# Performance work log

Measured on AMD Instinct MI355X. Metric: run time of the kernel, lower is better.

## Reference

```python
import jax, jax.numpy as jnp
import numpy as np

BATCH, ENC_IN, D_MODEL, D_STATE = 16, 256, 256, 16


def _mamba_params(key, d, d_conv, prefix):
    di = 2 * d  # expand = 2
    dtr = max(d // 16, 1)  # dt_rank = ceil(d_model/16)
    ks = jax.random.split(key, 6)
    return {
        prefix + '_in_w': jax.random.normal(ks[0], (2 * di, d), jnp.float32) * 0.02,
        prefix + '_conv_w': jax.random.normal(ks[1], (di, d_conv), jnp.float32) * 0.1,
        prefix + '_conv_b': jnp.zeros((di,), jnp.float32),
        prefix + '_xproj_w': jax.random.normal(ks[2], (dtr + 2 * D_STATE, di), jnp.float32) * 0.02,
        prefix + '_dt_w': jax.random.normal(ks[3], (di, dtr), jnp.float32) * 0.02,
        prefix + '_dt_b': jax.random.normal(ks[4], (di,), jnp.float32) * 0.02,
        prefix + '_Alog': jnp.log(jnp.broadcast_to(jnp.arange(1, D_STATE + 1, dtype=jnp.float32), (di, D_STATE))),
        prefix + '_Dp': jnp.ones((di,), jnp.float32),
        prefix + '_out_w': jax.random.normal(ks[5], (d, di), jnp.float32) * 0.02,
    }


def setup_inputs() -> dict:
    key = jax.random.key(0)
    k0, k1, k2, k3 = jax.random.split(key, 4)
    inp = {
        'x': jax.random.normal(k0, (BATCH, ENC_IN, D_MODEL), jnp.float32),
        'ln_g': jnp.ones((D_MODEL,), jnp.float32),
        'ln_b': jnp.zeros((D_MODEL,), jnp.float32),
    }
    inp.update(_mamba_params(k1, D_MODEL, 1, 'mf'))  # channel mixer fwd, d_conv=1
    inp.update(_mamba_params(k2, D_MODEL, 1, 'mb'))  # channel mixer bwd, d_conv=1
    inp.update(_mamba_params(k3, ENC_IN, 4, 'tm'))   # time mixer, d_conv=4
    return inp


def _mamba(x, in_w, conv_w, conv_b, xproj_w, dt_w, dt_b, Alog, Dp, out_w):
    # x: [B, L, d]  -> standard mamba_ssm Mamba block forward
    B, L, d = x.shape
    di = in_w.shape[0] // 2
    dtr = dt_w.shape[1]
    ds = D_STATE
    xz = x @ in_w.T                      # [B, L, 2*di]
    xs, z = xz[..., :di], xz[..., di:]
    # causal depthwise conv1d (pad left d_conv-1, truncate to L)
    K = conv_w.shape[1]
    xp = jnp.pad(xs, ((0, 0), (K - 1, 0), (0, 0)))
    xs = sum(conv_w[:, k] * xp[:, k:k + L, :] for k in range(K)) + conv_b
    xs = jax.nn.silu(xs)
    x_dbl = xs @ xproj_w.T               # [B, L, dtr + 2*ds]
    dt = x_dbl[..., :dtr]
    Bm = x_dbl[..., dtr:dtr + ds]        # [B, L, ds]
    Cm = x_dbl[..., dtr + ds:]           # [B, L, ds]
    delta = jax.nn.softplus(dt @ dt_w.T + dt_b)          # [B, L, di]
    A = -jnp.exp(Alog)                                   # [di, ds]
    dA = jnp.exp(delta[..., None] * A)                   # [B, L, di, ds]
    dBx = delta[..., None] * Bm[:, :, None, :] * xs[..., None]

    def step(h, inp):
        dAt, dBxt, Ct = inp              # [B,di,ds],[B,di,ds],[B,ds]
        h = dAt * h + dBxt
        return h, jnp.einsum('bds,bs->bd', h, Ct)

    h0 = jnp.zeros((B, di, ds), x.dtype)
    _, ys = jax.lax.scan(step, h0, (dA.transpose(1, 0, 2, 3), dBx.transpose(1, 0, 2, 3), Cm.transpose(1, 0, 2)))
    y = ys.transpose(1, 0, 2) + Dp * xs  # [B, L, di]
    y = y * jax.nn.silu(z)
    return y @ out_w.T                   # [B, L, d]


def _ln(x, g, b, eps=1e-5):
    m = x.mean(-1, keepdims=True)
    v = jnp.mean((x - m) ** 2, axis=-1, keepdims=True)
    return (x - m) / jnp.sqrt(v + eps) * g + b


def reference(x, ln_g, ln_b,
              mf_in_w, mf_conv_w, mf_conv_b, mf_xproj_w, mf_dt_w, mf_dt_b, mf_Alog, mf_Dp, mf_out_w,
              mb_in_w, mb_conv_w, mb_conv_b, mb_xproj_w, mb_dt_w, mb_dt_b, mb_Alog, mb_Dp, mb_out_w,
              tm_in_w, tm_conv_w, tm_conv_b, tm_xproj_w, tm_dt_w, tm_dt_b, tm_Alog, tm_Dp, tm_out_w):
    # BiMamba channel mixer
    y_f = _mamba(x, mf_in_w, mf_conv_w, mf_conv_b, mf_xproj_w, mf_dt_w, mf_dt_b, mf_Alog, mf_Dp, mf_out_w)
    y_b = _mamba(jnp.flip(x, axis=1), mb_in_w, mb_conv_w, mb_conv_b, mb_xproj_w, mb_dt_w, mb_dt_b, mb_Alog, mb_Dp, mb_out_w)
    y0 = y_f + jnp.flip(y_b, axis=1) + x
    y0 = _ln(y0, ln_g, ln_b)             # note: source uses norm1 both times
    # time mixer over the feature dimension
    y1 = y0.transpose(0, 2, 1)           # [B, d_model, enc_in]
    y1 = _mamba(y1, tm_in_w, tm_conv_w, tm_conv_b, tm_xproj_w, tm_dt_w, tm_dt_b, tm_Alog, tm_Dp, tm_out_w)
    y1 = y1.transpose(0, 2, 1)
    y2 = y1 * y0 + x
    return _ln(y2, ln_g, ln_b)
```

## Files before the change

kernel.cpp:

```cpp
#include <hip/hip_runtime.h>
#include <hip/hip_bf16.h>

typedef unsigned short u16;
typedef unsigned int   u32;

typedef short frag8 __attribute__((ext_vector_type(8)));
typedef float f32x4 __attribute__((ext_vector_type(4)));
typedef u16   u16x8 __attribute__((ext_vector_type(8)));
typedef u16   u16x4 __attribute__((ext_vector_type(4)));

__device__ __forceinline__ float bfb2f(u16 u) {
    return __uint_as_float(((u32)u) << 16);
}
__device__ __forceinline__ u16 f2bf(float v) {
    const u32 u = __float_as_uint(v);
    return (u16)((u + 0x7FFFu + ((u >> 16) & 1u)) >> 16);
}
__device__ __forceinline__ float silu_(float x) { return x / (1.f + __expf(-x)); }
__device__ __forceinline__ float softplus_fast(float x) {
    return (x > 20.f) ? x : __logf(1.f + __expf(x));
}
__device__ __forceinline__ void gload_lds16(const void* g, void* l) {
    __builtin_amdgcn_global_load_lds(
        (const __attribute__((address_space(1))) void*)g,
        (__attribute__((address_space(3))) void*)l, 16, 0, 0);
}

struct Cvt {
    const void* src[30];
    int dstoff[30];
    int n[30];
    int bstart[31];
};

__global__ __launch_bounds__(256) void convert_k(Cvt c, const u32* probe,
                                                 float* dst, u16* dstb) {
    const bool isb = (*probe != 0x3F800000u);
    const int bi = blockIdx.x;
    int i = 0;
    while (i < 29 && bi >= c.bstart[i + 1]) ++i;
    const int e = (bi - c.bstart[i]) * 256 + (int)threadIdx.x;
    if (e >= c.n[i]) return;
    const float v = isb ? bfb2f(((const u16*)c.src[i])[e])
                        : ((const float*)c.src[i])[e];
    dst[c.dstoff[i] + e]  = v;
    dstb[c.dstoff[i] + e] = f2bf(v);
}

__global__ __launch_bounds__(256, 4) void gemm1_fb_k(
    const u16* __restrict__ Xbf,
    const u16* __restrict__ Wf, const u16* __restrict__ Wb,
    const float* __restrict__ cwf, const float* __restrict__ cbf,
    const float* __restrict__ cwb, const float* __restrict__ cbb,
    u16* __restrict__ XSb_f, u16* __restrict__ XST_f, u16* __restrict__ ZST_f,
    u16* __restrict__ XSb_b, u16* __restrict__ XST_b, u16* __restrict__ ZST_b)
{
    __shared__ u16 Bs[16384];
    u16 (*tile)[136] = (u16(*)[136])Bs;

    const int br = blockIdx.x >> 4;
    const int n0 = (blockIdx.x & 15) * 64;
    const u16* W = br ? Wb : Wf;
    const float* cw = br ? cwb : cwf;
    const float* cb = br ? cbb : cbf;
    u16* XSb = br ? XSb_b : XSb_f;
    u16* XST = br ? XST_b : XST_f;
    u16* ZST = br ? ZST_b : ZST_f;

    const int t = threadIdx.x;
    const int wave = t >> 6, lane = t & 63;
    const int l15 = lane & 15, quad = lane >> 4;
    const int mblk = blockIdx.y * 128;

    {
        const char* Wp = (const char*)(W + (size_t)n0 * 256);
        const int lane16 = lane * 16;
        #pragma unroll
        for (int j = 0; j < 8; ++j) {
            const int s  = wave * 8 + j;
            const int Lb = s * 1024 + lane16;
            const int Ob = Lb ^ (((Lb >> 9) & 7) << 4);
            gload_lds16(Wp + Ob, (char*)Bs + Lb);
        }
    }
    asm volatile("s_waitcnt vmcnt(0)" ::: "memory");
    __syncthreads();

    const int m0w = mblk + wave * 32;
    const u16* arow0 = Xbf + (size_t)(m0w + l15) * 256 + quad * 8;
    const u16* arow1 = arow0 + 16 * 256;
    f32x4 acc[2][4] = {};
    #pragma unroll
    for (int kk = 0; kk < 8; ++kk) {
        const frag8 a0 = *(const frag8*)(arow0 + kk * 32);
        const frag8 a1 = *(const frag8*)(arow1 + kk * 32);
        #pragma unroll
        for (int ni = 0; ni < 4; ++ni) {
            const int bb = ((ni * 16 + l15) * 512 + kk * 64 + quad * 16)
                         ^ ((l15 & 7) << 4);
            const frag8 b = *(const frag8*)((const char*)Bs + bb);
            acc[0][ni] = __builtin_amdgcn_mfma_f32_16x16x32_bf16(a0, b, acc[0][ni], 0, 0, 0);
            acc[1][ni] = __builtin_amdgcn_mfma_f32_16x16x32_bf16(a1, b, acc[1][ni], 0, 0, 0);
        }
    }
    __syncthreads();

    const bool isx = (n0 < 512);
    #pragma unroll
    for (int mi = 0; mi < 2; ++mi) {
        #pragma unroll
        for (int ni = 0; ni < 4; ++ni) {
            const int n = n0 + ni * 16 + l15;
            #pragma unroll
            for (int r = 0; r < 4; ++r) {
                const int ml = wave * 32 + mi * 16 + quad * 4 + r;
                const int m  = mblk + ml;
                const float v = acc[mi][ni][r];
                const float s = isx ? silu_(fmaf(cw[n], v, cb[n])) : silu_(v);
                const u16 sb = f2bf(s);
                if (isx) XSb[(size_t)m * 512 + n] = sb;
                tile[ni * 16 + l15][ml] = sb;
            }
        }
    }
    __syncthreads();

    const int b2 = mblk >> 8;
    const int l0 = mblk & 255;
    const int rown = t >> 2;
    const int cc  = (t & 3) * 32;
    const int dg = isx ? (n0 + rown) : (n0 - 512 + rown);
    u16* dst = (isx ? XST : ZST) + ((size_t)(b2 * 512 + dg)) * 256 + l0 + cc;
    #pragma unroll
    for (int p = 0; p < 4; ++p)
        *(u16x8*)(dst + p * 8) = *(const u16x8*)&tile[rown][cc + p * 8];
}

__global__ __launch_bounds__(256, 4) void gemm1_tm_k(
    const u16* __restrict__ Ab, const u16* __restrict__ Bbg,
    float* __restrict__ TMRAW, u16* __restrict__ ZST)
{
    __shared__ u16 Bs[16384];
    u16 (*tile)[136] = (u16(*)[136])Bs;

    const int t = threadIdx.x;
    const int wave = t >> 6, lane = t & 63;
    const int l15 = lane & 15, quad = lane >> 4;
    const int mblk = blockIdx.y * 128;
    const int n0 = blockIdx.x * 64;

    {
        const char* Wp = (const char*)(Bbg + (size_t)n0 * 256);
        const int lane16 = lane * 16;
        #pragma unroll
        for (int j = 0; j < 8; ++j) {
            const int s  = wave * 8 + j;
            const int Lb = s * 1024 + lane16;
            const int Ob = Lb ^ (((Lb >> 9) & 7) << 4);
            gload_lds16(Wp + Ob, (char*)Bs + Lb);
        }
    }
    asm volatile("s_waitcnt vmcnt(0)" ::: "memory");
    __syncthreads();

    const int m0w = mblk + wave * 32;
    const u16* arow0 = Ab + (size_t)(m0w + l15) * 256 + quad * 8;
    const u16* arow1 = arow0 + 16 * 256;
    f32x4 acc[2][4] = {};
    #pragma unroll
    for (int kk = 0; kk < 8; ++kk) {
        const frag8 a0 = *(const frag8*)(arow0 + kk * 32);
        const frag8 a1 = *(const frag8*)(arow1 + kk * 32);
        #pragma unroll
        for (int ni = 0; ni < 4; ++ni) {
            const int bb = ((ni * 16 + l15) * 512 + kk * 64 + quad * 16)
                         ^ ((l15 & 7) << 4);
            const frag8 b = *(const frag8*)((const char*)Bs + bb);
            acc[0][ni] = __builtin_amdgcn_mfma_f32_16x16x32_bf16(a0, b, acc[0][ni], 0, 0, 0);
            acc[1][ni] = __builtin_amdgcn_mfma_f32_16x16x32_bf16(a1, b, acc[1][ni], 0, 0, 0);
        }
    }

    const bool isx = (n0 < 512);
    if (isx) {
        #pragma unroll
        for (int mi = 0; mi < 2; ++mi) {
            #pragma unroll
            for (int ni = 0; ni < 4; ++ni) {
                const int n = n0 + ni * 16 + l15;
                #pragma unroll
                for (int r = 0; r < 4; ++r) {
                    const int m = mblk + wave * 32 + mi * 16 + quad * 4 + r;
                    TMRAW[(size_t)m * 512 + n] = acc[mi][ni][r];
                }
            }
        }
    } else {
        __syncthreads();
        #pragma unroll
        for (int mi = 0; mi < 2; ++mi) {
            #pragma unroll
            for (int ni = 0; ni < 4; ++ni) {
                #pragma unroll
                for (int r = 0; r < 4; ++r) {
                    const int ml = wave * 32 + mi * 16 + quad * 4 + r;
                    tile[ni * 16 + l15][ml] = f2bf(silu_(acc[mi][ni][r]));
                }
            }
        }
        __syncthreads();
        const int b2 = mblk >> 8;
        const int l0 = mblk & 255;
        const int rown = t >> 2;
        const int cc  = (t & 3) * 32;
        u16* dst = ZST + ((size_t)(b2 * 512 + (n0 - 512) + rown)) * 256 + l0 + cc;
        #pragma unroll
        for (int p = 0; p < 4; ++p)
            *(u16x8*)(dst + p * 8) = *(const u16x8*)&tile[rown][cc + p * 8];
    }
}

__global__ __launch_bounds__(256, 2) void gemm_x_k(
    const u16* __restrict__ A0, const u16* __restrict__ B0, u16* __restrict__ O0,
    const u16* __restrict__ A1, const u16* __restrict__ B1, u16* __restrict__ O1)
{
    __shared__ char AB[81920];
    const int br = blockIdx.z;
    const u16* Ab = br ? A1 : A0;
    const u16* Bb = br ? B1 : B0;
    u16* out = br ? O1 : O0;
    const int t = threadIdx.x;
    const int wave = t >> 6, lane = t & 63;
    const int l15 = lane & 15, quad = lane >> 4;
    const int mblk = blockIdx.y * 64;
    const int n0 = blockIdx.x * 16;

    {
        const char* Ap = (const char*)(Ab + (size_t)mblk * 512);
        const char* Bp = (const char*)(Bb + (size_t)n0 * 512);
        const int lane16 = lane * 16;
        #pragma unroll
        for (int j = 0; j < 16; ++j) {
            const int Lb = (wave * 16 + j) * 1024 + lane16;
            const int Ob = Lb ^ (((Lb >> 10) & 7) << 4);
            gload_lds16(Ap + Ob, AB + Lb);
        }
        #pragma unroll
        for (int j = 0; j < 4; ++j) {
            const int Lb = (wave * 4 + j) * 1024 + lane16;
            const int Ob = Lb ^ (((Lb >> 10) & 7) << 4);
            gload_lds16(Bp + Ob, AB + 65536 + Lb);
        }
    }
    asm volatile("s_waitcnt vmcnt(0)" ::: "memory");
    __syncthreads();

    f32x4 acc = {};
    #pragma unroll
    for (int kk = 0; kk < 16; ++kk) {
        const int aoff = ((wave * 16 + l15) * 1024 + kk * 64 + quad * 16) ^ ((l15 & 7) << 4);
        const int boff = 65536 + ((l15 * 1024 + kk * 64 + quad * 16) ^ ((l15 & 7) << 4));
        const frag8 a = *(const frag8*)(AB + aoff);
        const frag8 b = *(const frag8*)(AB + boff);
        acc = __builtin_amdgcn_mfma_f32_16x16x32_bf16(a, b, acc, 0, 0, 0);
    }
    const int n = n0 + l15;
    const int m0 = mblk + wave * 16;
    #pragma unroll
    for (int r = 0; r < 4; ++r)
        out[(size_t)(m0 + quad * 4 + r) * 48 + n] = f2bf(acc[r]);
}

__global__ __launch_bounds__(256) void gemm_dt_k(
    const u16* __restrict__ A0, const u16* __restrict__ W0,
    const float* __restrict__ bias0, u16* __restrict__ O0,
    const u16* __restrict__ A1, const u16* __restrict__ W1,
    const float* __restrict__ bias1, u16* __restrict__ O1)
{
    __shared__ u16 tile[64][72];
    const int br = blockIdx.z;
    const u16* Ab = br ? A1 : A0;
    const u16* Wt = br ? W1 : W0;
    const float* bias = br ? bias1 : bias0;
    u16* out = br ? O1 : O0;

    const int t = threadIdx.x;
    const int wave = t >> 6, lane = t & 63;
    const int l15 = lane & 15, quad = lane >> 4;
    const int mblk = blockIdx.y * 64;
    const int m0 = mblk + wave * 16;
    const int n0 = blockIdx.x * 64;
    f32x4 acc[4] = {};
    frag8 a;
    #pragma unroll
    for (int j = 0; j < 8; ++j) a[j] = 0;
    if (quad < 2) a = *(const frag8*)(Ab + (size_t)(m0 + l15) * 48 + quad * 8);
    #pragma unroll
    for (int ni = 0; ni < 4; ++ni) {
        frag8 b;
        #pragma unroll
        for (int j = 0; j < 8; ++j) b[j] = 0;
        if (quad < 2) b = *(const frag8*)(Wt + (size_t)(n0 + ni * 16 + l15) * 16 + quad * 8);
        acc[ni] = __builtin_amdgcn_mfma_f32_16x16x32_bf16(a, b, acc[ni], 0, 0, 0);
    }
    #pragma unroll
    for (int ni = 0; ni < 4; ++ni) {
        const int n = n0 + ni * 16 + l15;
        #pragma unroll
        for (int r = 0; r < 4; ++r) {
            const int m = m0 + quad * 4 + r;
            tile[n - n0][m - mblk] = f2bf(softplus_fast(acc[ni][r] + bias[n]));
        }
    }
    __syncthreads();
    const int b  = mblk >> 8;
    const int l0 = mblk & 255;
    const int rown = t >> 2;
    const int chk  = (t & 3) * 16;
    u16* dst = out + ((size_t)(b * 512 + n0 + rown)) * 256 + l0 + chk;
    *(u16x8*)dst       = *(const u16x8*)&tile[rown][chk];
    *(u16x8*)(dst + 8) = *(const u16x8*)&tile[rown][chk + 8];
}

__global__ __launch_bounds__(256, 4) void gemm_o_k(
    const u16* __restrict__ A0, const u16* __restrict__ B0, float* __restrict__ O0,
    const u16* __restrict__ A1, const u16* __restrict__ B1, float* __restrict__ O1)
{
    __shared__ char Bs[32768];
    const int br = blockIdx.z;
    const u16* Ab = br ? A1 : A0;
    const u16* Bb = br ? B1 : B0;
    float* out = br ? O1 : O0;
    const int t = threadIdx.x;
    const int wave = t >> 6, lane = t & 63;
    const int l15 = lane & 15, quad = lane >> 4;
    const int mblk = blockIdx.y * 128;
    const int n0 = blockIdx.x * 32;

    {
        const char* Bp = (const char*)(Bb + (size_t)n0 * 512);
        const int lane16 = lane * 16;
        #pragma unroll
        for (int j = 0; j < 8; ++j) {
            const int Lb = (wave * 8 + j) * 1024 + lane16;
            const int Ob = Lb ^ (((Lb >> 10) & 7) << 4);
            gload_lds16(Bp + Ob, Bs + Lb);
        }
    }
    asm volatile("s_waitcnt vmcnt(0)" ::: "memory");
    __syncthreads();

    const int m0w = mblk + wave * 32;
    const u16* arow0 = Ab + (size_t)(m0w + l15) * 512 + quad * 8;
    const u16* arow1 = arow0 + 16 * 512;
    f32x4 acc[2][2] = {};
    #pragma unroll
    for (int kk = 0; kk < 16; ++kk) {
        const frag8 a0 = *(const frag8*)(arow0 + kk * 32);
        const frag8 a1 = *(const frag8*)(arow1 + kk * 32);
        #pragma unroll
        for (int ni = 0; ni < 2; ++ni) {
            const int boff = ((ni * 16 + l15) * 1024 + kk * 64 + quad * 16) ^ ((l15 & 7) << 4);
            const frag8 b = *(const frag8*)(Bs + boff);
            acc[0][ni] = __builtin_amdgcn_mfma_f32_16x16x32_bf16(a0, b, acc[0][ni], 0, 0, 0);
            acc[1][ni] = __builtin_amdgcn_mfma_f32_16x16x32_bf16(a1, b, acc[1][ni], 0, 0, 0);
        }
    }
    #pragma unroll
    for (int mi = 0; mi < 2; ++mi) {
        #pragma unroll
        for (int ni = 0; ni < 2; ++ni) {
            const int n = n0 + ni * 16 + l15;
            #pragma unroll
            for (int r = 0; r < 4; ++r) {
                const int m = mblk + wave * 32 + mi * 16 + quad * 4 + r;
                out[(size_t)m * 256 + n] = acc[mi][ni][r];
            }
        }
    }
}

__global__ __launch_bounds__(256) void conv4t_k(
    const float* __restrict__ raw, const float* __restrict__ cw, const float* __restrict__ cb,
    u16* __restrict__ XSb, u16* __restrict__ XST)
{
    __shared__ u16 tile[64][72];
    const int b  = blockIdx.y;
    const int c0 = blockIdx.x * 64;
    const int cl = threadIdx.x & 63;
    const int seg = threadIdx.x >> 6;
    const int c = c0 + cl;
    const int tq = blockIdx.z * 64;
    const int tp0 = tq + seg * 16;
    const float w0 = cw[c * 4 + 0], w1 = cw[c * 4 + 1];
    const float w2 = cw[c * 4 + 2], w3 = cw[c * 4 + 3];
    const float bias = cb[c];
    float r3 = 0.f, r2 = 0.f, r1 = 0.f;
    if (tp0 > 0) {
        r3 = raw[((size_t)(b * 256 + tp0 - 3)) * 512 + c];
        r2 = raw[((size_t)(b * 256 + tp0 - 2)) * 512 + c];
        r1 = raw[((size_t)(b * 256 + tp0 - 1)) * 512 + c];
    }
    #pragma unroll
    for (int i = 0; i < 16; ++i) {
        const int tp = tp0 + i;
        const float cur = raw[((size_t)(b * 256 + tp)) * 512 + c];
        float acc = fmaf(w0, r3, bias);
        acc = fmaf(w1, r2, acc);
        acc = fmaf(w2, r1, acc);
        acc = fmaf(w3, cur, acc);
        const u16 sb = f2bf(silu_(acc));
        XSb[((size_t)(b * 256 + tp)) * 512 + c] = sb;
        tile[cl][tp - tq] = sb;
        r3 = r2; r2 = r1; r1 = cur;
    }
    __syncthreads();
    const int row = threadIdx.x >> 2;
    const int ch  = (threadIdx.x & 3) * 16;
    u16* dst = XST + ((size_t)(b * 512 + c0 + row)) * 256 + tq + ch;
    #pragma unroll
    for (int j = 0; j < 4; ++j)
        *(u16x4*)(dst + j * 4) = *(const u16x4*)&tile[row][ch + j * 4];
}

struct ScanSet {
    const u16 *xst, *zst, *dlt, *xdblb;
    const float *Alog, *Dp;
    u16* Y;
};

__global__ __launch_bounds__(256) void scan_fused_k(ScanSet s0, ScanSet s1, int branchStart)
{
    __shared__ float Ps[4354];
    __shared__ float Es[4354];
    const int br  = (blockIdx.x >= (u32)branchStart) ? 1 : 0;
    const ScanSet S = br ? s1 : s0;
    const int rev = br;
    const int bi2 = blockIdx.x - br * branchStart;
    const int b  = bi2 >> 6;
    const int d0 = (bi2 & 63) << 3;
    const int g  = threadIdx.x >> 3;
    const int cl = threadIdx.x & 7;
    const int d  = d0 + cl;

    bool fast = true;
    #pragma unroll
    for (int s = 0; s < 16; ++s) {
        const float a = -__expf(S.Alog[d * 16 + s]);
        fast &= (fabsf(a + (float)(s + 1)) < 1e-3f);
    }

    const size_t crow = ((size_t)(b * 512 + d)) * 256;
    const int lbase = rev ? (248 - g * 8) : (g * 8);
    const u16x8 xs8 = *(const u16x8*)(S.xst + crow + lbase);
    const u16x8 dl8 = *(const u16x8*)(S.dlt + crow + lbase);

    float h[16], P[16];
    #pragma unroll
    for (int s = 0; s < 16; ++s) { h[s] = 0.f; P[s] = 1.f; }
    float e1prod = 1.f;

    #pragma unroll
    for (int i = 0; i < 8; ++i) {
        const int j = rev ? (7 - i) : i;
        const int l = lbase + j;
        const size_t row = (size_t)(b * 256 + l);
        const float dl = bfb2f(dl8[j]);
        const float xv = bfb2f(xs8[j]);
        const u16x8 bv0 = *(const u16x8*)(S.xdblb + row * 48 + 16);
        const u16x8 bv1 = *(const u16x8*)(S.xdblb + row * 48 + 24);
        const float dlx = dl * xv;
        if (fast) {
            const float e1 = __expf(-dl);
            e1prod *= e1;
            const float e2 = e1 * e1, e4 = e2 * e2, e8 = e4 * e4;
            float pw[16];
            pw[0] = e1;        pw[1] = e2;        pw[2] = e2 * e1;   pw[3] = e4;
            pw[4] = e4 * e1;   pw[5] = e4 * e2;   pw[6] = e4 * pw[2]; pw[7] = e8;
            pw[8] = e8 * e1;   pw[9] = e8 * e2;   pw[10] = e8 * pw[2]; pw[11] = e8 * e4;
            pw[12] = e8 * pw[4]; pw[13] = e8 * pw[5]; pw[14] = e8 * pw[6]; pw[15] = e8 * e8;
            #pragma unroll
            for (int s = 0; s < 8; ++s)
                h[s] = fmaf(pw[s], h[s], dlx * bfb2f(bv0[s]));
            #pragma unroll
            for (int s = 8; s < 16; ++s)
                h[s] = fmaf(pw[s], h[s], dlx * bfb2f(bv1[s - 8]));
        } else {
            #pragma unroll
            for (int s = 0; s < 16; ++s) {
                const float As = -__expf(S.Alog[d * 16 + s]);
                const float dA = __expf(dl * As);
                P[s] *= dA;
                const float Bv = bfb2f((s < 8) ? bv0[s] : bv1[s - 8]);
                h[s] = fmaf(dA, h[s], dlx * Bv);
            }
        }
    }
    if (fast) {
        const float e1 = e1prod;
        const float e2 = e1 * e1, e4 = e2 * e2, e8 = e4 * e4;
        P[0] = e1;        P[1] = e2;        P[2] = e2 * e1;   P[3] = e4;
        P[4] = e4 * e1;   P[5] = e4 * e2;   P[6] = e4 * P[2]; P[7] = e8;
        P[8] = e8 * e1;   P[9] = e8 * e2;   P[10] = e8 * P[2]; P[11] = e8 * e4;
        P[12] = e8 * P[4]; P[13] = e8 * P[5]; P[14] = e8 * P[6]; P[15] = e8 * e8;
    }
    const int pbx = (g * 8 + cl) * 17;
    #pragma unroll
    for (int s = 0; s < 16; ++s) { Ps[pbx + s] = P[s]; Es[pbx + s] = h[s]; }
    __syncthreads();

    if (threadIdx.x < 128) {
        const int cl2 = threadIdx.x >> 4, s2 = threadIdx.x & 15;
        float hh = 0.f;
        #pragma unroll
        for (int gg = 0; gg < 32; ++gg) {
            const int o = (gg * 8 + cl2) * 17 + s2;
            const float tmp = Es[o];
            Es[o] = hh;
            hh = fmaf(Ps[o], hh, tmp);
        }
    }
    __syncthreads();

    #pragma unroll
    for (int s = 0; s < 16; ++s) h[s] = Es[pbx + s];
    const float Dpd = S.Dp[d];
    const u16x8 zs8 = *(const u16x8*)(S.zst + crow + lbase);
    #pragma unroll
    for (int i = 0; i < 8; ++i) {
        const int j = rev ? (7 - i) : i;
        const int l = lbase + j;
        const size_t row = (size_t)(b * 256 + l);
        const float dl = bfb2f(dl8[j]);
        const float xv = bfb2f(xs8[j]);
        const float zv = bfb2f(zs8[j]);
        const u16x8 bv0 = *(const u16x8*)(S.xdblb + row * 48 + 16);
        const u16x8 bv1 = *(const u16x8*)(S.xdblb + row * 48 + 24);
        const u16x8 cv0 = *(const u16x8*)(S.xdblb + row * 48 + 32);
        const u16x8 cv1 = *(const u16x8*)(S.xdblb + row * 48 + 40);
        const float dlx = dl * xv;
        float a0 = 0.f, a1 = 0.f, a2 = 0.f, a3 = 0.f;
        if (fast) {
            const float e1 = __expf(-dl);
            const float e2 = e1 * e1, e4 = e2 * e2, e8 = e4 * e4;
            float pw[16];
            pw[0] = e1;        pw[1] = e2;        pw[2] = e2 * e1;   pw[3] = e4;
            pw[4] = e4 * e1;   pw[5] = e4 * e2;   pw[6] = e4 * pw[2]; pw[7] = e8;
            pw[8] = e8 * e1;   pw[9] = e8 * e2;   pw[10] = e8 * pw[2]; pw[11] = e8 * e4;
            pw[12] = e8 * pw[4]; pw[13] = e8 * pw[5]; pw[14] = e8 * pw[6]; pw[15] = e8 * e8;
            #pragma unroll
            for (int s = 0; s < 16; ++s) {
                const float Bv = bfb2f((s < 8) ? bv0[s] : bv1[s - 8]);
                const float Cv = bfb2f((s < 8) ? cv0[s] : cv1[s - 8]);
                h[s] = fmaf(pw[s], h[s], dlx * Bv);
                const float hv = h[s] * Cv;
                if ((s & 3) == 0) a0 += hv;
                else if ((s & 3) == 1) a1 += hv;
                else if ((s & 3) == 2) a2 += hv;
                else a3 += hv;
            }
        } else {
            #pragma unroll
            for (int s = 0; s < 16; ++s) {
                const float As = -__expf(S.Alog[d * 16 + s]);
                const float dA = __expf(dl * As);
                const float Bv = bfb2f((s < 8) ? bv0[s] : bv1[s - 8]);
                const float Cv = bfb2f((s < 8) ? cv0[s] : cv1[s - 8]);
                h[s] = fmaf(dA, h[s], dlx * Bv);
                const float hv = h[s] * Cv;
                if ((s & 3) == 0) a0 += hv;
                else if ((s & 3) == 1) a1 += hv;
                else if ((s & 3) == 2) a2 += hv;
                else a3 += hv;
            }
        }
        const float acc = (a0 + a1) + (a2 + a3);
        S.Y[row * 512 + d] = f2bf((acc + Dpd * xv) * zv);
    }
}

__global__ __launch_bounds__(256) void combine_ln_k(
    const float* __restrict__ YF, const float* __restrict__ YB,
    const float* __restrict__ X, const float* __restrict__ g, const float* __restrict__ bb,
    float* __restrict__ Y0, u16* __restrict__ Y0T)
{
    const int m = blockIdx.x;
    const int c = threadIdx.x;
    const float v = YF[(size_t)m * 256 + c]
                  + YB[(size_t)m * 256 + c]
                  + X[(size_t)m * 256 + c];
    float s1 = v, s2 = v * v;
    #pragma unroll
    for (int off = 32; off > 0; off >>= 1) {
        s1 += __shfl_down(s1, off);
        s2 += __shfl_down(s2, off);
    }
    __shared__ float p1[4], p2[4];
    const int wave = c >> 6;
    if ((c & 63) == 0) { p1[wave] = s1; p2[wave] = s2; }
    __syncthreads();
    const float t1 = (p1[0] + p1[1]) + (p1[2] + p1[3]);
    const float t2 = (p2[0] + p2[1]) + (p2[2] + p2[3]);
    const float mean = t1 * (1.f / 256.f);
    const float var  = t2 * (1.f / 256.f) - mean * mean;
    const float inv  = rsqrtf(var + 1e-5f);
    const float o = (v - mean) * inv * g[c] + bb[c];
    Y0[(size_t)m * 256 + c] = o;
    const int b2 = m >> 8, l = m & 255;
    Y0T[((size_t)(b2 * 256 + c)) * 256 + l] = f2bf(o);
}

__global__ __launch_bounds__(256) void final_ln_k(
    const float* __restrict__ TMOUT, const float* __restrict__ Y0,
    const float* __restrict__ X, const float* __restrict__ g, const float* __restrict__ bb,
    float* __restrict__ out)
{
    const int m = blockIdx.x;
    const int c = threadIdx.x;
    const int b = m >> 8, l = m & 255;
    const float y1 = TMOUT[((size_t)(b * 256 + c)) * 256 + l];
    const float v = fmaf(y1, Y0[(size_t)m * 256 + c], X[(size_t)m * 256 + c]);
    float s1 = v, s2 = v * v;
    #pragma unroll
    for (int off = 32; off > 0; off >>= 1) {
        s1 += __shfl_down(s1, off);
        s2 += __shfl_down(s2, off);
    }
    __shared__ float p1[4], p2[4];
    const int wave = c >> 6;
    if ((c & 63) == 0) { p1[wave] = s1; p2[wave] = s2; }
    __syncthreads();
    const float t1 = (p1[0] + p1[1]) + (p1[2] + p1[3]);
    const float t2 = (p2[0] + p2[1]) + (p2[2] + p2[3]);
    const float mean = t1 * (1.f / 256.f);
    const float var  = t2 * (1.f / 256.f) - mean * mean;
    const float inv  = rsqrtf(var + 1e-5f);
    out[(size_t)m * 256 + c] = (v - mean) * inv * g[c] + bb[c];
}

extern "C" void kernel_launch(void* const* d_in, const int* in_sizes, int n_in,
                              void* d_out, int out_size, void* d_ws, size_t ws_size,
                              hipStream_t stream)
{
    float* ws = (float*)d_ws;

    Cvt c;
    int off = 0, blocks = 0;
    int doff[30];
    for (int i = 0; i < 30; ++i) {
        c.src[i]    = d_in[i];
        c.dstoff[i] = off;
        doff[i]     = off;
        c.n[i]      = in_sizes[i];
        c.bstart[i] = blocks;
        off    += in_sizes[i];
        blocks += (in_sizes[i] + 255) / 256;
    }
    c.bstart[30] = blocks;
    const int offa = (off + 7) & ~7;
    float* PARF = ws;
    u16*   PARB = (u16*)(ws + offa);
    float* ACT0 = ws + offa + offa / 2;

    convert_k<<<dim3(blocks), dim3(256), 0, stream>>>(c, (const u32*)d_in[1], PARF, PARB);

    auto P  = [&](int base, int o) -> const float* { return PARF + doff[base + o]; };
    auto Pb = [&](int base, int o) -> const u16*   { return PARB + doff[base + o]; };
    const float* X   = P(0, 0);
    const u16*   Xbf = Pb(0, 0);
    const float* lng = P(1, 0);
    const float* lnb = P(2, 0);

    u16* XSb_f   = (u16*)ACT0;
    u16* XSb_b   = XSb_f + 2097152;
    u16* XST_f   = XSb_b + 2097152;
    u16* XST_b   = XST_f + 2097152;
    u16* ZST_f   = XST_b + 2097152;
    u16* ZST_b   = ZST_f + 2097152;
    u16* DLT_f   = ZST_b + 2097152;
    u16* DLT_b   = DLT_f + 2097152;
    u16* Ybf_f   = DLT_b + 2097152;
    u16* Ybf_b   = Ybf_f + 2097152;
    u16* XDBLb_f = Ybf_b + 2097152;
    u16* XDBLb_b = XDBLb_f + 196608;
    u16* Y0T     = XDBLb_b + 196608;
    float* Y0    = (float*)(Y0T + 1048576);
    float* YF    = Y0 + 1048576;
    float* YB    = YF + 1048576;
    float* TMRAW = YB + 1048576;
    float* TMOUT = TMRAW + 2097152;

    const dim3 blk(256);
    const int mf = 3, mb = 12, tm = 21;

    gemm1_fb_k<<<dim3(32, 32), blk, 0, stream>>>(
        Xbf, Pb(mf, 0), Pb(mb, 0),
        P(mf, 1), P(mf, 2), P(mb, 1), P(mb, 2),
        XSb_f, XST_f, ZST_f, XSb_b, XST_b, ZST_b);
    gemm_x_k<<<dim3(3, 64, 2), blk, 0, stream>>>(
        XSb_f, Pb(mf, 3), XDBLb_f, XSb_b, Pb(mb, 3), XDBLb_b);
    gemm_dt_k<<<dim3(8, 64, 2), blk, 0, stream>>>(
        XDBLb_f, Pb(mf, 4), P(mf, 5), DLT_f,
        XDBLb_b, Pb(mb, 4), P(mb, 5), DLT_b);
    {
        ScanSet s0 { XST_f, ZST_f, DLT_f, XDBLb_f, P(mf, 6), P(mf, 7), Ybf_f };
        ScanSet s1 { XST_b, ZST_b, DLT_b, XDBLb_b, P(mb, 6), P(mb, 7), Ybf_b };
        scan_fused_k<<<dim3(2048), blk, 0, stream>>>(s0, s1, 1024);
    }
    gemm_o_k<<<dim3(8, 32, 2), blk, 0, stream>>>(
        Ybf_f, Pb(mf, 8), YF, Ybf_b, Pb(mb, 8), YB);

    combine_ln_k<<<dim3(4096), blk, 0, stream>>>(YF, YB, X, lng, lnb, Y0, Y0T);

    gemm1_tm_k<<<dim3(16, 32), blk, 0, stream>>>(Y0T, Pb(tm, 0), TMRAW, ZST_f);
    conv4t_k<<<dim3(8, 16, 4), blk, 0, stream>>>(TMRAW, P(tm, 1), P(tm, 2), XSb_f, XST_f);
    gemm_x_k<<<dim3(3, 64, 1), blk, 0, stream>>>(
        XSb_f, Pb(tm, 3), XDBLb_f, XSb_f, Pb(tm, 3), XDBLb_f);
    gemm_dt_k<<<dim3(8, 64, 1), blk, 0, stream>>>(
        XDBLb_f, Pb(tm, 4), P(tm, 5), DLT_f,
        XDBLb_f, Pb(tm, 4), P(tm, 5), DLT_f);
    {
        ScanSet t0 { XST_f, ZST_f, DLT_f, XDBLb_f, P(tm, 6), P(tm, 7), Ybf_f };
        scan_fused_k<<<dim3(1024), blk, 0, stream>>>(t0, t0, 2048);
    }
    gemm_o_k<<<dim3(8, 32, 1), blk, 0, stream>>>(
        Ybf_f, Pb(tm, 8), TMOUT, Ybf_f, Pb(tm, 8), TMOUT);

    final_ln_k<<<dim3(4096), blk, 0, stream>>>(TMOUT, Y0, X, lng, lnb, (float*)d_out);
}
```

Baseline: 265.4 us.

## Fuse x_proj GEMM with dt projection and softplus into one kernel

```diff
diff --git a/kernel.cpp b/kernel.cpp
--- a/kernel.cpp
+++ b/kernel.cpp
@@ -220,15 +220,22 @@
     }
 }
 
-__global__ __launch_bounds__(256, 2) void gemm_x_k(
-    const u16* __restrict__ A0, const u16* __restrict__ B0, u16* __restrict__ O0,
-    const u16* __restrict__ A1, const u16* __restrict__ B1, u16* __restrict__ O1)
-{
-    __shared__ char AB[81920];
+__global__ __launch_bounds__(256, 2) void gemm_xdt_k(
+    const u16* __restrict__ A0, const u16* __restrict__ B0,
+    const u16* __restrict__ W0, const float* __restrict__ bias0,
+    u16* __restrict__ O0, u16* __restrict__ D0,
+    const u16* __restrict__ A1, const u16* __restrict__ B1,
+    const u16* __restrict__ W1, const float* __restrict__ bias1,
+    u16* __restrict__ O1, u16* __restrict__ D1)
+{
+    __shared__ __align__(16) char AB[81920];
     const int br = blockIdx.z;
     const u16* Ab = br ? A1 : A0;
     const u16* Bb = br ? B1 : B0;
+    const u16* Wt = br ? W1 : W0;
+    const float* bias = br ? bias1 : bias0;
     u16* out = br ? O1 : O0;
+    u16* DLT = br ? D1 : D0;
     const int t = threadIdx.x;
     const int wave = t >> 6, lane = t & 63;
     const int l15 = lane & 15, quad = lane >> 4;
@@ -264,62 +271,71 @@
         const frag8 b = *(const frag8*)(AB + boff);
         acc = __builtin_amdgcn_mfma_f32_16x16x32_bf16(a, b, acc, 0, 0, 0);
     }
-    const int n = n0 + l15;
     const int m0 = mblk + wave * 16;
+
+    if (blockIdx.x != 0) {
+        const int n = n0 + l15;
+        #pragma unroll
+        for (int r = 0; r < 4; ++r)
+            out[(size_t)(m0 + quad * 4 + r) * 48 + n] = f2bf(acc[r]);
+        return;
+    }
+
+    __syncthreads();
+    u16* dtT = (u16*)AB;
     #pragma unroll
     for (int r = 0; r < 4; ++r)
-        out[(size_t)(m0 + quad * 4 + r) * 48 + n] = f2bf(acc[r]);
-}
-
-__global__ __launch_bounds__(256) void gemm_dt_k(
-    const u16* __restrict__ A0, const u16* __restrict__ W0,
-    const float* __restrict__ bias0, u16* __restrict__ O0,
-    const u16* __restrict__ A1, const u16* __restrict__ W1,
-    const float* __restrict__ bias1, u16* __restrict__ O1)
-{
-    __shared__ u16 tile[64][72];
-    const int br = blockIdx.z;
-    const u16* Ab = br ? A1 : A0;
-    const u16* Wt = br ? W1 : W0;
-    const float* bias = br ? bias1 : bias0;
-    u16* out = br ? O1 : O0;
-
-    const int t = threadIdx.x;
-    const int wave = t >> 6, lane = t & 63;
-    const int l15 = lane & 15, quad = lane >> 4;
-    const int mblk = blockIdx.y * 64;
-    const int m0 = mblk + wave * 16;
-    const int n0 = blockIdx.x * 64;
-    f32x4 acc[4] = {};
-    frag8 a;
-    #pragma unroll
-    for (int j = 0; j < 8; ++j) a[j] = 0;
-    if (quad < 2) a = *(const frag8*)(Ab + (size_t)(m0 + l15) * 48 + quad * 8);
-    #pragma unroll
-    for (int ni = 0; ni < 4; ++ni) {
-        frag8 b;
-        #pragma unroll
-        for (int j = 0; j < 8; ++j) b[j] = 0;
-        if (quad < 2) b = *(const frag8*)(Wt + (size_t)(n0 + ni * 16 + l15) * 16 + quad * 8);
-        acc[ni] = __builtin_amdgcn_mfma_f32_16x16x32_bf16(a, b, acc[ni], 0, 0, 0);
-    }
-    #pragma unroll
-    for (int ni = 0; ni < 4; ++ni) {
-        const int n = n0 + ni * 16 + l15;
-        #pragma unroll
-        for (int r = 0; r < 4; ++r) {
-            const int m = m0 + quad * 4 + r;
-            tile[n - n0][m - mblk] = f2bf(softplus_fast(acc[ni][r] + bias[n]));
-        }
-    }
-    __syncthreads();
-    const int b  = mblk >> 8;
+        dtT[(wave * 16 + quad * 4 + r) * 24 + l15] = f2bf(acc[r]);
+    {
+        const char* Wp = (const char*)Wt;
+        #pragma unroll
+        for (int j = 0; j < 4; ++j) {
+            const int Lb = (wave * 4 + j) * 1024 + lane * 16;
+            gload_lds16(Wp + Lb, AB + 4096 + Lb);
+        }
+    }
+    asm volatile("s_waitcnt vmcnt(0)" ::: "memory");
+    __syncthreads();
+
+    frag8 a2;
+    #pragma unroll
+    for (int j = 0; j < 8; ++j) a2[j] = 0;
+    if (quad < 2)
+        a2 = *(const frag8*)(dtT + (wave * 16 + l15) * 24 + quad * 8);
+
+    const u16* dtwL = (const u16*)(AB + 4096);
+    u16 (*tile)[72] = (u16(*)[72])(AB + 20480);
+    const int gb = mblk >> 8;
     const int l0 = mblk & 255;
     const int rown = t >> 2;
     const int chk  = (t & 3) * 16;
-    u16* dst = out + ((size_t)(b * 512 + n0 + rown)) * 256 + l0 + chk;
-    *(u16x8*)dst       = *(const u16x8*)&tile[rown][chk];
-    *(u16x8*)(dst + 8) = *(const u16x8*)&tile[rown][chk + 8];
+    #pragma unroll
+    for (int nblk = 0; nblk < 8; ++nblk) {
+        f32x4 acc2[4] = {};
+        #pragma unroll
+        for (int nt = 0; nt < 4; ++nt) {
+            frag8 b2;
+            #pragma unroll
+            for (int j = 0; j < 8; ++j) b2[j] = 0;
+            if (quad < 2)
+                b2 = *(const frag8*)(dtwL + (nblk * 64 + nt * 16 + l15) * 16 + quad * 8);
+            acc2[nt] = __builtin_amdgcn_mfma_f32_16x16x32_bf16(a2, b2, acc2[nt], 0, 0, 0);
+        }
+        __syncthreads();
+        #pragma unroll
+        for (int nt = 0; nt < 4; ++nt) {
+            #pragma unroll
+            for (int r = 0; r < 4; ++r) {
+                const int n = nblk * 64 + nt * 16 + l15;
+                tile[nt * 16 + l15][wave * 16 + quad * 4 + r]
+                    = f2bf(softplus_fast(acc2[nt][r] + bias[n]));
+            }
+        }
+        __syncthreads();
+        u16* dst = DLT + ((size_t)(gb * 512 + nblk * 64 + rown)) * 256 + l0 + chk;
+        *(u16x8*)dst       = *(const u16x8*)&tile[rown][chk];
+        *(u16x8*)(dst + 8) = *(const u16x8*)&tile[rown][chk + 8];
+    }
 }
 
 __global__ __launch_bounds__(256, 4) void gemm_o_k(
@@ -697,11 +713,9 @@
         Xbf, Pb(mf, 0), Pb(mb, 0),
         P(mf, 1), P(mf, 2), P(mb, 1), P(mb, 2),
         XSb_f, XST_f, ZST_f, XSb_b, XST_b, ZST_b);
-    gemm_x_k<<<dim3(3, 64, 2), blk, 0, stream>>>(
-        XSb_f, Pb(mf, 3), XDBLb_f, XSb_b, Pb(mb, 3), XDBLb_b);
-    gemm_dt_k<<<dim3(8, 64, 2), blk, 0, stream>>>(
-        XDBLb_f, Pb(mf, 4), P(mf, 5), DLT_f,
-        XDBLb_b, Pb(mb, 4), P(mb, 5), DLT_b);
+    gemm_xdt_k<<<dim3(3, 64, 2), blk, 0, stream>>>(
+        XSb_f, Pb(mf, 3), Pb(mf, 4), P(mf, 5), XDBLb_f, DLT_f,
+        XSb_b, Pb(mb, 3), Pb(mb, 4), P(mb, 5), XDBLb_b, DLT_b);
     {
         ScanSet s0 { XST_f, ZST_f, DLT_f, XDBLb_f, P(mf, 6), P(mf, 7), Ybf_f };
         ScanSet s1 { XST_b, ZST_b, DLT_b, XDBLb_b, P(mb, 6), P(mb, 7), Ybf_b };
@@ -714,11 +728,9 @@
 
     gemm1_tm_k<<<dim3(16, 32), blk, 0, stream>>>(Y0T, Pb(tm, 0), TMRAW, ZST_f);
     conv4t_k<<<dim3(8, 16, 4), blk, 0, stream>>>(TMRAW, P(tm, 1), P(tm, 2), XSb_f, XST_f);
-    gemm_x_k<<<dim3(3, 64, 1), blk, 0, stream>>>(
-        XSb_f, Pb(tm, 3), XDBLb_f, XSb_f, Pb(tm, 3), XDBLb_f);
-    gemm_dt_k<<<dim3(8, 64, 1), blk, 0, stream>>>(
-        XDBLb_f, Pb(tm, 4), P(tm, 5), DLT_f,
-        XDBLb_f, Pb(tm, 4), P(tm, 5), DLT_f);
+    gemm_xdt_k<<<dim3(3, 64, 1), blk, 0, stream>>>(
+        XSb_f, Pb(tm, 3), Pb(tm, 4), P(tm, 5), XDBLb_f, DLT_f,
+        XSb_f, Pb(tm, 3), Pb(tm, 4), P(tm, 5), XDBLb_f, DLT_f);
     {
         ScanSet t0 { XST_f, ZST_f, DLT_f, XDBLb_f, P(tm, 6), P(tm, 7), Ybf_f };
         scan_fused_k<<<dim3(1024), blk, 0, stream>>>(t0, t0, 2048);
```

Measured after the change: 276.5 us. +4.2%, slower.
